# Kernel tuning notes

Measured on AMD Instinct MI355X. Metric: run time of the kernel, lower is better.

Reference implementation:

```python
import jax, jax.numpy as jnp
import numpy as np

V, N = 3, 32768
C2, C3 = 256, 32          # feat_ch_2D, feat_ch_3D
H = W = 128               # 2D feature map size
D = 32                    # 3D volume feature size
CIN = C2 + C3             # 288, MLP in_channels


def setup_inputs() -> dict:
    key = jax.random.key(0)
    ks = jax.random.split(key, 16)
    sc = 0.02
    inp = {
        'pts': jax.random.uniform(ks[0], (1, N, 3), minval=-0.5, maxval=0.5),
        'pts_proj': jax.random.uniform(ks[1], (1, N, 2), minval=-1.0, maxval=1.0),
        'img_feat0': jax.random.normal(ks[2], (V, C2, H, W)),
        'img_feat1': jax.random.normal(ks[3], (V, C2, H, W)),
        'vol_feat0': jax.random.normal(ks[4], (V, C3, D, D, D)),
        'vol_feat1': jax.random.normal(ks[5], (V, C3, D, D, D)),
        'W0': jax.random.normal(ks[6], (1024, CIN)) * sc,  'b0': jnp.zeros((1024,)),
        'W1': jax.random.normal(ks[7], (512, CIN + 1024)) * sc, 'b1': jnp.zeros((512,)),
        'W2': jax.random.normal(ks[8], (256, CIN + 512)) * sc,  'b2': jnp.zeros((256,)),
        'W3': jax.random.normal(ks[9], (128, CIN + 256)) * sc,  'b3': jnp.zeros((128,)),
        'W4': jax.random.normal(ks[10], (1, 128)) * sc,         'b4': jnp.zeros((1,)),
        'mean_num': 3,
    }
    return inp


def _gs2d(feat, gx, gy):
    # feat: [C,H,W]; gx,gy: [N] normalized coords in [-1,1]
    C, Hh, Ww = feat.shape
    ix = jnp.clip(((gx + 1.0) * Ww - 1.0) * 0.5, 0.0, Ww - 1.0)  # align_corners=False, border pad
    iy = jnp.clip(((gy + 1.0) * Hh - 1.0) * 0.5, 0.0, Hh - 1.0)
    x0f, y0f = jnp.floor(ix), jnp.floor(iy)
    wx, wy = ix - x0f, iy - y0f
    x0 = x0f.astype(jnp.int32); x1 = jnp.minimum(x0 + 1, Ww - 1)
    y0 = y0f.astype(jnp.int32); y1 = jnp.minimum(y0 + 1, Hh - 1)
    v00 = feat[:, y0, x0]; v01 = feat[:, y0, x1]
    v10 = feat[:, y1, x0]; v11 = feat[:, y1, x1]
    return (v00 * (1 - wy) * (1 - wx) + v01 * (1 - wy) * wx
            + v10 * wy * (1 - wx) + v11 * wy * wx)  # [C,N]


def _gs3d(feat, gx, gy, gz):
    # feat: [C,D,H,W]; grid x->W, y->H, z->D (torch grid_sample convention)
    C, Dd, Hh, Ww = feat.shape
    ix = jnp.clip(((gx + 1.0) * Ww - 1.0) * 0.5, 0.0, Ww - 1.0)
    iy = jnp.clip(((gy + 1.0) * Hh - 1.0) * 0.5, 0.0, Hh - 1.0)
    iz = jnp.clip(((gz + 1.0) * Dd - 1.0) * 0.5, 0.0, Dd - 1.0)
    x0f, y0f, z0f = jnp.floor(ix), jnp.floor(iy), jnp.floor(iz)
    wx, wy, wz = ix - x0f, iy - y0f, iz - z0f
    x0 = x0f.astype(jnp.int32); x1 = jnp.minimum(x0 + 1, Ww - 1)
    y0 = y0f.astype(jnp.int32); y1 = jnp.minimum(y0 + 1, Hh - 1)
    z0 = z0f.astype(jnp.int32); z1 = jnp.minimum(z0 + 1, Dd - 1)
    def g(zi, yi, xi):
        return feat[:, zi, yi, xi]  # [C,N]
    out = (g(z0, y0, x0) * (1 - wz) * (1 - wy) * (1 - wx)
           + g(z0, y0, x1) * (1 - wz) * (1 - wy) * wx
           + g(z0, y1, x0) * (1 - wz) * wy * (1 - wx)
           + g(z0, y1, x1) * (1 - wz) * wy * wx
           + g(z1, y0, x0) * wz * (1 - wy) * (1 - wx)
           + g(z1, y0, x1) * wz * (1 - wy) * wx
           + g(z1, y1, x0) * wz * wy * (1 - wx)
           + g(z1, y1, x1) * wz * wy * wx)
    return out  # [C,N]


def _lrelu(x):
    return jnp.where(x >= 0, x, 0.2 * x)


def _conv1x1(Wm, bm, x):
    # x: [V,C,N] -> [V,O,N]
    return jnp.einsum('oc,vcn->von', Wm, x) + bm[None, :, None]


def _mlp0(x, W0, b0, W1, b1, W2, b2, W3, b3):
    out = _lrelu(_conv1x1(W0, b0, x))
    out = _lrelu(_conv1x1(W1, b1, jnp.concatenate([x, out], axis=1)))
    out = _lrelu(_conv1x1(W2, b2, jnp.concatenate([x, out], axis=1)))
    out = _lrelu(_conv1x1(W3, b3, jnp.concatenate([x, out], axis=1)))
    return out  # [V,128,N]


def _forward(pts, pts_proj, img_feats, vol_feats,
             W0, b0, W1, b1, W2, b2, W3, b3, W4, b4, mean_num):
    v = img_feats[0].shape[0]
    gx2 = jnp.broadcast_to(pts_proj[:, :, 0], (v, pts_proj.shape[1]))
    gy2 = jnp.broadcast_to(pts_proj[:, :, 1], (v, pts_proj.shape[1]))
    p = pts * 2.0  # pts *= 2.0 before 3D sampling
    gx3 = jnp.broadcast_to(p[:, :, 0], (v, p.shape[1]))
    gy3 = jnp.broadcast_to(p[:, :, 1], (v, p.shape[1]))
    gz3 = jnp.broadcast_to(p[:, :, 2], (v, p.shape[1]))
    outs = []
    for img_feat, vol_feat in zip(img_feats, vol_feats):
        f2 = jax.vmap(_gs2d)(img_feat, gx2, gy2)            # [V,C2,N]
        f3 = jax.vmap(_gs3d)(vol_feat, gx3, gy3, gz3)       # [V,C3,N]
        pt_feat = jnp.concatenate([f2, f3], axis=1)         # [V,288,N]
        pt_out0 = _mlp0(pt_feat, W0, b0, W1, b1, W2, b2, W3, b3)
        pt_out0_mean = jnp.mean(pt_out0[:mean_num], axis=0, keepdims=True)  # [1,128,N]
        sdf = jax.nn.sigmoid(_conv1x1(W4, b4, pt_out0_mean))                # [1,1,N]
        outs.append(jnp.transpose(sdf, (0, 2, 1)))                          # [1,N,1]
    return tuple(outs)


def reference(pts, pts_proj, img_feat0, img_feat1, vol_feat0, vol_feat1,
              W0, b0, W1, b1, W2, b2, W3, b3, W4, b4, mean_num):
    return _forward(pts, pts_proj, [img_feat0, img_feat1], [vol_feat0, vol_feat1],
                    W0, b0, W1, b1, W2, b2, W3, b3, W4, b4, mean_num)
```

## Files before the change

kernel.cpp:

```cpp
#include <hip/hip_runtime.h>
#include <hip/hip_bf16.h>

#define NV 3
#define NPTS 32768
#define C2C 256
#define C3C 32
#define CINC 288
#define CINP 320
#define HH 128
#define WWW 128
#define DDD 32

typedef short bh8 __attribute__((ext_vector_type(8)));
typedef float fx4 __attribute__((ext_vector_type(4)));
typedef unsigned short us4 __attribute__((ext_vector_type(4)));

__device__ __forceinline__ float b2f(unsigned short u) {
    unsigned int x = ((unsigned int)u) << 16;
    return __uint_as_float(x);
}
__device__ __forceinline__ unsigned short f2b(float f) {
    unsigned int x = __float_as_uint(f);
    unsigned int r = (x + 0x7FFFu + ((x >> 16) & 1u)) >> 16;
    return (unsigned short)r;
}

__device__ __forceinline__ void gl2lds16(const unsigned short* g, unsigned short* l) {
    __builtin_amdgcn_global_load_lds(
        (const __attribute__((address_space(1))) unsigned int*)g,
        (__attribute__((address_space(3))) unsigned int*)l, 16, 0, 0);
}

__device__ __forceinline__ int xcd_swz(int orig, int nwg) {
    int xcd = orig & 7;
    int q = nwg >> 3, r = nwg & 7;
    int base = (xcd < r) ? xcd * (q + 1) : r * (q + 1) + (xcd - r) * q;
    return base + (orig >> 3);
}

__global__ void k_wpad(const float* __restrict__ src, unsigned short* __restrict__ dst, int M, int Kp) {
    int idx = blockIdx.x * 256 + threadIdx.x;
    if (idx >= M * Kp) return;
    int m = idx / Kp, k = idx - m * Kp;
    int Ksrc = Kp - 32;
    float v;
    if (k < CINC) v = src[(size_t)m * Ksrc + k];
    else if (k < CINP) v = 0.0f;
    else v = src[(size_t)m * Ksrc + (k - 32)];
    dst[idx] = f2b(v);
}

__global__ void k_timg(const float* __restrict__ in, unsigned short* __restrict__ out) {
    int v = blockIdx.x >> 7, y = blockIdx.x & 127;
    int x0 = blockIdx.y << 6, c0 = blockIdx.z << 6;
    __shared__ float t[64][65];
    int tx = threadIdx.x & 63, tg = threadIdx.x >> 6;
    const float* src = in + (((size_t)(v * C2C + c0) * HH + y) * WWW + x0);
#pragma unroll
    for (int i = 0; i < 16; i++) {
        int cl = tg * 16 + i;
        t[cl][tx] = src[(size_t)cl * (HH * WWW) + tx];
    }
    __syncthreads();
    unsigned short* dst = out + ((size_t)(v * HH + y) * WWW + x0) * C2C + c0;
#pragma unroll
    for (int i = 0; i < 16; i++) {
        int xl = tg * 16 + i;
        dst[(size_t)xl * C2C + tx] = f2b(t[tx][xl]);
    }
}

__global__ void k_tvol(const float* __restrict__ in, unsigned short* __restrict__ out) {
    int v = blockIdx.x;
    int s0 = blockIdx.y << 8;
    __shared__ float t[32][257];
    int tid = threadIdx.x;
    const float* src = in + (size_t)v * C3C * 32768 + s0;
#pragma unroll
    for (int c = 0; c < 32; c++) t[c][tid] = src[(size_t)c * 32768 + tid];
    __syncthreads();
    unsigned short* dst = out + ((size_t)v * 32768 + s0) * C3C;
    int c = tid & 31, sb = tid >> 5;
#pragma unroll
    for (int j = 0; j < 32; j++) {
        int sl = j * 8 + sb;
        dst[(size_t)sl * C3C + c] = f2b(t[c][sl]);
    }
}

__global__ __launch_bounds__(256) void k_sample(const float* __restrict__ pts, const float* __restrict__ proj,
                         const unsigned short* __restrict__ imgT, const unsigned short* __restrict__ volT,
                         unsigned short* __restrict__ ptT, int n0, int Nk) {
    int w = threadIdx.x >> 6, l = threadIdx.x & 63;
    int i = blockIdx.x * 4 + w;
    int v = blockIdx.y;
    int n = n0 + i;
    unsigned short* dstRow = ptT + (size_t)(v * Nk + i) * CINP;

    {
        float gx = proj[n * 2 + 0], gy = proj[n * 2 + 1];
        float ix = fminf(fmaxf(((gx + 1.0f) * (float)WWW - 1.0f) * 0.5f, 0.0f), (float)(WWW - 1));
        float iy = fminf(fmaxf(((gy + 1.0f) * (float)HH - 1.0f) * 0.5f, 0.0f), (float)(HH - 1));
        float x0f = floorf(ix), y0f = floorf(iy);
        float wx = ix - x0f, wy = iy - y0f;
        int x0 = (int)x0f, y0 = (int)y0f;
        int x1 = min(x0 + 1, WWW - 1), y1 = min(y0 + 1, HH - 1);
        const unsigned short* base = imgT + (size_t)v * HH * WWW * C2C;
        us4 a = *((const us4*)(base + ((size_t)(y0 * WWW + x0)) * C2C) + l);
        us4 b = *((const us4*)(base + ((size_t)(y0 * WWW + x1)) * C2C) + l);
        us4 c = *((const us4*)(base + ((size_t)(y1 * WWW + x0)) * C2C) + l);
        us4 d = *((const us4*)(base + ((size_t)(y1 * WWW + x1)) * C2C) + l);
        float w00 = (1.0f - wy) * (1.0f - wx), w01 = (1.0f - wy) * wx;
        float w10 = wy * (1.0f - wx), w11 = wy * wx;
        us4 rv;
#pragma unroll
        for (int r = 0; r < 4; r++) {
            float f = b2f(a[r]) * w00 + b2f(b[r]) * w01 + b2f(c[r]) * w10 + b2f(d[r]) * w11;
            rv[r] = f2b(f);
        }
        *(us4*)(dstRow + l * 4) = rv;
    }
    {
        float gx = pts[n * 3 + 0] * 2.0f, gy = pts[n * 3 + 1] * 2.0f, gz = pts[n * 3 + 2] * 2.0f;
        float ix = fminf(fmaxf(((gx + 1.0f) * (float)DDD - 1.0f) * 0.5f, 0.0f), (float)(DDD - 1));
        float iy = fminf(fmaxf(((gy + 1.0f) * (float)DDD - 1.0f) * 0.5f, 0.0f), (float)(DDD - 1));
        float iz = fminf(fmaxf(((gz + 1.0f) * (float)DDD - 1.0f) * 0.5f, 0.0f), (float)(DDD - 1));
        float x0f = floorf(ix), y0f = floorf(iy), z0f = floorf(iz);
        float wx = ix - x0f, wy = iy - y0f, wz = iz - z0f;
        int x0 = (int)x0f, y0 = (int)y0f, z0 = (int)z0f;
        int x1 = min(x0 + 1, DDD - 1), y1 = min(y0 + 1, DDD - 1), z1 = min(z0 + 1, DDD - 1);
        int c = l & 31, zs = l >> 5;
        int zi = zs ? z1 : z0;
        float wzs = zs ? wz : (1.0f - wz);
        const unsigned short* base = volT + (size_t)v * 32768 * C3C;
        float f00 = b2f(base[((size_t)((zi * 32 + y0) * 32 + x0)) * C3C + c]);
        float f01 = b2f(base[((size_t)((zi * 32 + y0) * 32 + x1)) * C3C + c]);
        float f10 = b2f(base[((size_t)((zi * 32 + y1) * 32 + x0)) * C3C + c]);
        float f11 = b2f(base[((size_t)((zi * 32 + y1) * 32 + x1)) * C3C + c]);
        float r = (f00 * (1.0f - wy) * (1.0f - wx) + f01 * (1.0f - wy) * wx +
                   f10 * wy * (1.0f - wx) + f11 * wy * wx) * wzs;
        float other = __shfl_xor(r, 32);
        r += other;
        if (zs == 0) dstRow[C2C + c] = f2b(r);
    }
    if (l < 8) *(us4*)(dstRow + CINC + l * 4) = (us4){0, 0, 0, 0};
}

template <int K1, int K2, int M>
__device__ __forceinline__ void gemm128_body(const unsigned short* __restrict__ A,
                                             const unsigned short* __restrict__ B1,
                                             const unsigned short* __restrict__ B2,
                                             const float* __restrict__ bias,
                                             unsigned short* __restrict__ C) {
    constexpr int K = K1 + K2;
    __shared__ unsigned short Ash[128 * 32];
    __shared__ unsigned short Bsh[128 * 32];
    int tid = threadIdx.x;
    int w = tid >> 6, l = tid & 63;
    int la = l & 15, lg = l >> 4;
    int wm = w & 1, wn = w >> 1;
    int gx = gridDim.x;
    int nwg = gx * gridDim.y;
    int bid = xcd_swz(blockIdx.y * gx + blockIdx.x, nwg);
    int mBlk = (bid % gx) * 128;
    int nBlk = (bid / gx) * 128;

    int sRow = l >> 2;
    int sCol = (l & 3) * 8;

    fx4 acc[4][4];
#pragma unroll
    for (int mi = 0; mi < 4; mi++)
#pragma unroll
        for (int ni = 0; ni < 4; ni++) acc[mi][ni] = (fx4){0.f, 0.f, 0.f, 0.f};

    const unsigned short* Ag = A + (size_t)mBlk * K;
    {
        const unsigned short* Bg = B1 + (size_t)nBlk * K1;
        for (int k0 = 0; k0 < K1; k0 += 32) {
#pragma unroll
            for (int j = 0; j < 2; j++) {
                int r = w * 32 + j * 16 + sRow;
                gl2lds16(Ag + (size_t)r * K + k0 + sCol, &Ash[r * 32 + sCol]);
                gl2lds16(Bg + (size_t)r * K1 + k0 + sCol, &Bsh[r * 32 + sCol]);
            }
            __syncthreads();
            bh8 af[4], bfv[4];
#pragma unroll
            for (int mi = 0; mi < 4; mi++) af[mi] = *(const bh8*)&Ash[(wm * 64 + mi * 16 + la) * 32 + lg * 8];
#pragma unroll
            for (int ni = 0; ni < 4; ni++) bfv[ni] = *(const bh8*)&Bsh[(wn * 64 + ni * 16 + la) * 32 + lg * 8];
#pragma unroll
            for (int mi = 0; mi < 4; mi++)
#pragma unroll
                for (int ni = 0; ni < 4; ni++)
                    acc[mi][ni] = __builtin_amdgcn_mfma_f32_16x16x32_bf16(af[mi], bfv[ni], acc[mi][ni], 0, 0, 0);
            __syncthreads();
        }
    }
    if constexpr (K2 > 0) {
        const unsigned short* Bg = B2 + (size_t)nBlk * K2;
        for (int k0 = 0; k0 < K2; k0 += 32) {
#pragma unroll
            for (int j = 0; j < 2; j++) {
                int r = w * 32 + j * 16 + sRow;
                gl2lds16(Ag + (size_t)r * K + K1 + k0 + sCol, &Ash[r * 32 + sCol]);
                gl2lds16(Bg + (size_t)r * K2 + k0 + sCol, &Bsh[r * 32 + sCol]);
            }
            __syncthreads();
            bh8 af[4], bfv[4];
#pragma unroll
            for (int mi = 0; mi < 4; mi++) af[mi] = *(const bh8*)&Ash[(wm * 64 + mi * 16 + la) * 32 + lg * 8];
#pragma unroll
            for (int ni = 0; ni < 4; ni++) bfv[ni] = *(const bh8*)&Bsh[(wn * 64 + ni * 16 + la) * 32 + lg * 8];
#pragma unroll
            for (int mi = 0; mi < 4; mi++)
#pragma unroll
                for (int ni = 0; ni < 4; ni++)
                    acc[mi][ni] = __builtin_amdgcn_mfma_f32_16x16x32_bf16(af[mi], bfv[ni], acc[mi][ni], 0, 0, 0);
            __syncthreads();
        }
    }

#pragma unroll
    for (int mi = 0; mi < 4; mi++) {
        int m0 = mBlk + wm * 64 + mi * 16 + lg * 4;
        fx4 bb = *(const fx4*)(bias + m0);
#pragma unroll
        for (int ni = 0; ni < 4; ni++) {
            int n = nBlk + wn * 64 + ni * 16 + la;
            us4 rv;
#pragma unroll
            for (int r = 0; r < 4; r++) {
                float x = acc[mi][ni][r] + bb[r];
                x = (x >= 0.0f) ? x : 0.2f * x;
                rv[r] = f2b(x);
            }
            *(us4*)(C + (size_t)n * M + m0) = rv;
        }
    }
}

__global__ __launch_bounds__(256) void k_g0(const unsigned short* __restrict__ A, const unsigned short* __restrict__ B1,
                                            const float* __restrict__ bias, unsigned short* __restrict__ C) {
    gemm128_body<320, 0, 1024>(A, B1, nullptr, bias, C);
}
__global__ __launch_bounds__(256) void k_g2(const unsigned short* __restrict__ A, const unsigned short* __restrict__ B1,
                                            const unsigned short* __restrict__ B2, const float* __restrict__ bias,
                                            unsigned short* __restrict__ C) {
    gemm128_body<320, 512, 256>(A, B1, B2, bias, C);
}
__global__ __launch_bounds__(256) void k_g3(const unsigned short* __restrict__ A, const unsigned short* __restrict__ B1,
                                            const unsigned short* __restrict__ B2, const float* __restrict__ bias,
                                            unsigned short* __restrict__ C) {
    gemm128_body<320, 256, 128>(A, B1, B2, bias, C);
}

__global__ __launch_bounds__(512) void k_g1(const unsigned short* __restrict__ A,
                                            const unsigned short* __restrict__ B1,
                                            const unsigned short* __restrict__ B2,
                                            const float* __restrict__ bias,
                                            unsigned short* __restrict__ C) {
    constexpr int Kp = 1344;
    constexpr int K2 = 1024;
    constexpr int M = 512;
    constexpr int nt = Kp >> 6;
    __shared__ unsigned short As[2][256 * 64];
    __shared__ unsigned short Bs[2][256 * 64];
    int tid = threadIdx.x;
    int w = tid >> 6, l = tid & 63;
    int la = l & 15, lg = l >> 4;
    int wm = w >> 2, wn = w & 3;
    int g = wn >> 1;
    int gx = gridDim.x;
    int nwg = gx * gridDim.y;
    int bid = xcd_swz(blockIdx.y * gx + blockIdx.x, nwg);
    int mBlk = (bid % gx) * 256;
    int nBlk = (bid / gx) * 256;

    const unsigned short* Ag = A + (size_t)mBlk * Kp;

    fx4 acc[8][4];
#pragma unroll
    for (int mi = 0; mi < 8; mi++)
#pragma unroll
        for (int ni = 0; ni < 4; ni++) acc[mi][ni] = (fx4){0.f, 0.f, 0.f, 0.f};

    auto burst = [&](int t, int nxt) {
        const unsigned short* bsrc;
        size_t ldb;
        int kc;
        if (t < 5) { bsrc = B1; ldb = CINP; kc = t * 64; }
        else       { bsrc = B2; ldb = (size_t)K2; kc = (t - 5) * 64; }
        bsrc += (size_t)nBlk * ldb + kc;
        const unsigned short* asrc = Ag + t * 64;
#pragma unroll
        for (int h = 0; h < 2; h++)
#pragma unroll
            for (int j = 0; j < 2; j++) {
                int idx = j * 512 + tid;
                int r = (h << 7) + (idx >> 3);
                int c = (idx & 7) ^ (r & 7);
                gl2lds16(asrc + (size_t)r * Kp + c * 8, &As[nxt][(h << 13) + idx * 8]);
            }
#pragma unroll
        for (int h = 0; h < 2; h++)
#pragma unroll
            for (int j = 0; j < 2; j++) {
                int idx = j * 512 + tid;
                int r = (h << 7) + (idx >> 3);
                int c = (idx & 7) ^ (r & 7);
                gl2lds16(bsrc + (size_t)r * ldb + c * 8, &Bs[nxt][(h << 13) + idx * 8]);
            }
    };

    burst(0, 0);
    for (int t = 0; t < nt; t++) {
        int cur = t & 1;
        if (t + 1 < nt) {
            burst(t + 1, cur ^ 1);
            if (g == 0) asm volatile("s_waitcnt vmcnt(10)" ::: "memory");
            else        asm volatile("s_waitcnt vmcnt(8)" ::: "memory");
        } else {
            if (g == 0) asm volatile("s_waitcnt vmcnt(2)" ::: "memory");
            else        asm volatile("s_waitcnt vmcnt(0)" ::: "memory");
        }
        const unsigned short* Ab = &As[cur][0];
        const unsigned short* Bb = &Bs[cur][0];
        bh8 afr[4][2];
#pragma unroll
        for (int p = 0; p < 4; p++) {
            int qm = p >> 1, qn = p & 1;
            if (qn == 0) {
#pragma unroll
                for (int m2 = 0; m2 < 4; m2++)
#pragma unroll
                    for (int s = 0; s < 2; s++) {
                        int row = wm * 128 + (qm * 4 + m2) * 16 + la;
                        int c = (s * 4 + lg) ^ (row & 7);
                        afr[m2][s] = *(const bh8*)&Ab[row * 64 + c * 8];
                    }
            }
            bh8 bfr[2][2];
#pragma unroll
            for (int n2 = 0; n2 < 2; n2++)
#pragma unroll
                for (int s = 0; s < 2; s++) {
                    int row = wn * 64 + (qn * 2 + n2) * 16 + la;
                    int c = (s * 4 + lg) ^ (row & 7);
                    bfr[n2][s] = *(const bh8*)&Bb[row * 64 + c * 8];
                }
            __builtin_amdgcn_s_barrier();
            __builtin_amdgcn_s_setprio(1);
#pragma unroll
            for (int m2 = 0; m2 < 4; m2++)
#pragma unroll
                for (int n2 = 0; n2 < 2; n2++)
#pragma unroll
                    for (int s = 0; s < 2; s++)
                        acc[qm * 4 + m2][qn * 2 + n2] = __builtin_amdgcn_mfma_f32_16x16x32_bf16(
                            afr[m2][s], bfr[n2][s], acc[qm * 4 + m2][qn * 2 + n2], 0, 0, 0);
            __builtin_amdgcn_s_setprio(0);
            if (p == 3) asm volatile("s_waitcnt lgkmcnt(0)" ::: "memory");
            __builtin_amdgcn_s_barrier();
        }
    }

#pragma unroll
    for (int mi = 0; mi < 8; mi++) {
        int m0 = mBlk + wm * 128 + mi * 16 + lg * 4;
        fx4 bb = *(const fx4*)(bias + m0);
#pragma unroll
        for (int ni = 0; ni < 4; ni++) {
            int n = nBlk + wn * 64 + ni * 16 + la;
            us4 rv;
#pragma unroll
            for (int r = 0; r < 4; r++) {
                float x = acc[mi][ni][r] + bb[r];
                x = (x >= 0.0f) ? x : 0.2f * x;
                rv[r] = f2b(x);
            }
            *(us4*)(C + (size_t)n * M + m0) = rv;
        }
    }
}

__global__ void k_head(const unsigned short* __restrict__ o3, const float* __restrict__ W4,
                       const float* __restrict__ b4, const int* __restrict__ mn_p,
                       float* __restrict__ out, int n0, int Nk, int level) {
    int i = blockIdx.x * 256 + threadIdx.x;
    if (i >= Nk) return;
    int mn = *mn_p;
    if (mn > NV) mn = NV;
    if (mn < 1) mn = 1;
    float s = 0.0f;
    for (int v = 0; v < mn; v++) {
        const unsigned short* row = o3 + (size_t)(v * Nk + i) * 128;
        for (int c0 = 0; c0 < 128; c0 += 8) {
            bh8 x = *(const bh8*)(row + c0);
#pragma unroll
            for (int r = 0; r < 8; r++) s += W4[c0 + r] * b2f((unsigned short)x[r]);
        }
    }
    s = s / (float)mn + b4[0];
    out[(size_t)level * NPTS + n0 + i] = 1.0f / (1.0f + expf(-s));
}

extern "C" void kernel_launch(void* const* d_in, const int* in_sizes, int n_in,
                              void* d_out, int out_size, void* d_ws, size_t ws_size,
                              hipStream_t stream) {
    const float* pts = (const float*)d_in[0];
    const float* proj = (const float*)d_in[1];
    const float* img[2] = {(const float*)d_in[2], (const float*)d_in[3]};
    const float* vol[2] = {(const float*)d_in[4], (const float*)d_in[5]};
    const float* Wf[4] = {(const float*)d_in[6], (const float*)d_in[8], (const float*)d_in[10], (const float*)d_in[12]};
    const float* bf[4] = {(const float*)d_in[7], (const float*)d_in[9], (const float*)d_in[11], (const float*)d_in[13]};
    const float* W4 = (const float*)d_in[14];
    const float* b4 = (const float*)d_in[15];
    const int* mn = (const int*)d_in[16];
    float* out = (float*)d_out;

    const int Kp[4] = {320, 1344, 832, 576};
    const int Msz[4] = {1024, 512, 256, 128};

    char* ws = (char*)d_ws;
    size_t off = 0;
    auto alloc = [&](size_t bytes) -> char* {
        char* p = ws + off;
        off = (off + bytes + 255) & ~(size_t)255;
        return p;
    };

    unsigned short* Wb[4];
    for (int i = 0; i < 4; i++) Wb[i] = (unsigned short*)alloc((size_t)Msz[i] * Kp[i] * 2);
    unsigned short* imgT = (unsigned short*)alloc((size_t)NV * HH * WWW * C2C * 2);
    unsigned short* volT = (unsigned short*)alloc((size_t)NV * 32768 * C3C * 2);
    size_t fixed = off;

    const size_t perPt = (size_t)NV * 2 * (CINP + 1024 + 512 + 256 + 128);
    int Nk = NPTS;
    if (fixed + (size_t)Nk * perPt + 4096 > ws_size) {
        size_t avail = (ws_size > fixed + 4096) ? (ws_size - fixed - 4096) : 0;
        long nk = (long)(avail / perPt);
        nk = (nk / 256) * 256;
        if (nk < 256) nk = 256;
        if (nk > NPTS) nk = NPTS;
        Nk = (int)nk;
    }
    unsigned short* ptT = (unsigned short*)alloc((size_t)NV * Nk * CINP * 2);
    unsigned short* o0 = (unsigned short*)alloc((size_t)NV * Nk * 1024 * 2);
    unsigned short* o1 = (unsigned short*)alloc((size_t)NV * Nk * 512 * 2);
    unsigned short* o2 = (unsigned short*)alloc((size_t)NV * Nk * 256 * 2);
    unsigned short* o3 = (unsigned short*)alloc((size_t)NV * Nk * 128 * 2);

    for (int i = 0; i < 4; i++) {
        int n = Msz[i] * Kp[i];
        k_wpad<<<(n + 255) / 256, 256, 0, stream>>>(Wf[i], Wb[i], Msz[i], Kp[i]);
    }

    for (int lvl = 0; lvl < 2; lvl++) {
        k_timg<<<dim3(NV * HH, WWW / 64, C2C / 64), 256, 0, stream>>>(img[lvl], imgT);
        k_tvol<<<dim3(NV, 32768 / 256), 256, 0, stream>>>(vol[lvl], volT);
        for (int n0 = 0; n0 < NPTS; n0 += Nk) {
            int nk = NPTS - n0 < Nk ? NPTS - n0 : Nk;
            int NC = NV * nk;
            k_sample<<<dim3(nk / 4, NV), 256, 0, stream>>>(pts, proj, imgT, volT, ptT, n0, nk);
            k_g0<<<dim3(1024 / 128, NC / 128), 256, 0, stream>>>(Wb[0], ptT, bf[0], o0);
            k_g1<<<dim3(512 / 256, NC / 256), 512, 0, stream>>>(Wb[1], ptT, o0, bf[1], o1);
            k_g2<<<dim3(256 / 128, NC / 128), 256, 0, stream>>>(Wb[2], ptT, o1, bf[2], o2);
            k_g3<<<dim3(128 / 128, NC / 128), 256, 0, stream>>>(Wb[3], ptT, o2, bf[3], o3);
            k_head<<<(nk + 255) / 256, 256, 0, stream>>>(o3, W4, b4, mn, out, n0, nk, lvl);
        }
    }
}
```

Before: 1.079 ms.

## Reschedule k_g1 prefetch, split its launch in halves, parallelize head reduction

The k_g1 GEMM now issues the next tile's global-to-LDS burst after the first MFMA sub-step instead of before compute, with one uniform vmcnt wait before the final barrier. It is also launched as two half-grid kernels using a column offset. The head kernel now gives each point 16 lanes, each doing a slice of the 128-channel dot product, then combines them with a shuffle reduction, so more threads run and loads coalesce. Splitting k_g1 adds a launch and may leave the GPU partly idle at the tail, and the new wait placement changes load/compute overlap.

```diff
diff --git a/kernel.cpp b/kernel.cpp
--- a/kernel.cpp
+++ b/kernel.cpp
@@ -260,7 +260,7 @@
                                             const unsigned short* __restrict__ B1,
                                             const unsigned short* __restrict__ B2,
                                             const float* __restrict__ bias,
-                                            unsigned short* __restrict__ C) {
+                                            unsigned short* __restrict__ C, int nOff) {
     constexpr int Kp = 1344;
     constexpr int K2 = 1024;
     constexpr int M = 512;
@@ -271,12 +271,11 @@
     int w = tid >> 6, l = tid & 63;
     int la = l & 15, lg = l >> 4;
     int wm = w >> 2, wn = w & 3;
-    int g = wn >> 1;
     int gx = gridDim.x;
     int nwg = gx * gridDim.y;
     int bid = xcd_swz(blockIdx.y * gx + blockIdx.x, nwg);
     int mBlk = (bid % gx) * 256;
-    int nBlk = (bid / gx) * 256;
+    int nBlk = (bid / gx) * 256 + nOff;
 
     const unsigned short* Ag = A + (size_t)mBlk * Kp;
 
@@ -315,16 +314,10 @@
     };
 
     burst(0, 0);
+    asm volatile("s_waitcnt vmcnt(0)" ::: "memory");
+    __builtin_amdgcn_s_barrier();
     for (int t = 0; t < nt; t++) {
         int cur = t & 1;
-        if (t + 1 < nt) {
-            burst(t + 1, cur ^ 1);
-            if (g == 0) asm volatile("s_waitcnt vmcnt(10)" ::: "memory");
-            else        asm volatile("s_waitcnt vmcnt(8)" ::: "memory");
-        } else {
-            if (g == 0) asm volatile("s_waitcnt vmcnt(2)" ::: "memory");
-            else        asm volatile("s_waitcnt vmcnt(0)" ::: "memory");
-        }
         const unsigned short* Ab = &As[cur][0];
         const unsigned short* Bb = &Bs[cur][0];
         bh8 afr[4][2];
@@ -361,7 +354,11 @@
                         acc[qm * 4 + m2][qn * 2 + n2] = __builtin_amdgcn_mfma_f32_16x16x32_bf16(
                             afr[m2][s], bfr[n2][s], acc[qm * 4 + m2][qn * 2 + n2], 0, 0, 0);
             __builtin_amdgcn_s_setprio(0);
-            if (p == 3) asm volatile("s_waitcnt lgkmcnt(0)" ::: "memory");
+            if (p == 0 && t + 1 < nt) burst(t + 1, cur ^ 1);
+            if (p == 3) {
+                asm volatile("s_waitcnt lgkmcnt(0)" ::: "memory");
+                if (t + 1 < nt) asm volatile("s_waitcnt vmcnt(8)" ::: "memory");
+            }
             __builtin_amdgcn_s_barrier();
         }
     }
@@ -385,25 +382,32 @@
     }
 }
 
-__global__ void k_head(const unsigned short* __restrict__ o3, const float* __restrict__ W4,
+__global__ __launch_bounds__(256) void k_head(const unsigned short* __restrict__ o3, const float* __restrict__ W4,
                        const float* __restrict__ b4, const int* __restrict__ mn_p,
                        float* __restrict__ out, int n0, int Nk, int level) {
-    int i = blockIdx.x * 256 + threadIdx.x;
+    int wv = threadIdx.x >> 6, l = threadIdx.x & 63;
+    int sub = l >> 4, cl = l & 15;
+    int i = blockIdx.x * 16 + wv * 4 + sub;
     if (i >= Nk) return;
     int mn = *mn_p;
     if (mn > NV) mn = NV;
     if (mn < 1) mn = 1;
+    fx4 w0 = *(const fx4*)(W4 + cl * 8);
+    fx4 w1 = *(const fx4*)(W4 + cl * 8 + 4);
     float s = 0.0f;
     for (int v = 0; v < mn; v++) {
-        const unsigned short* row = o3 + (size_t)(v * Nk + i) * 128;
-        for (int c0 = 0; c0 < 128; c0 += 8) {
-            bh8 x = *(const bh8*)(row + c0);
-#pragma unroll
-            for (int r = 0; r < 8; r++) s += W4[c0 + r] * b2f((unsigned short)x[r]);
-        }
-    }
-    s = s / (float)mn + b4[0];
-    out[(size_t)level * NPTS + n0 + i] = 1.0f / (1.0f + expf(-s));
+        bh8 x = *(const bh8*)(o3 + (size_t)(v * Nk + i) * 128 + cl * 8);
+#pragma unroll
+        for (int r = 0; r < 4; r++) s += w0[r] * b2f((unsigned short)x[r]);
+#pragma unroll
+        for (int r = 0; r < 4; r++) s += w1[r] * b2f((unsigned short)x[4 + r]);
+    }
+#pragma unroll
+    for (int m = 1; m < 16; m <<= 1) s += __shfl_xor(s, m);
+    if (cl == 0) {
+        s = s / (float)mn + b4[0];
+        out[(size_t)level * NPTS + n0 + i] = 1.0f / (1.0f + expf(-s));
+    }
 }
 
 extern "C" void kernel_launch(void* const* d_in, const int* in_sizes, int n_in,
@@ -442,8 +446,8 @@
     if (fixed + (size_t)Nk * perPt + 4096 > ws_size) {
         size_t avail = (ws_size > fixed + 4096) ? (ws_size - fixed - 4096) : 0;
         long nk = (long)(avail / perPt);
-        nk = (nk / 256) * 256;
-        if (nk < 256) nk = 256;
+        nk = (nk / 512) * 512;
+        if (nk < 512) nk = 512;
         if (nk > NPTS) nk = NPTS;
         Nk = (int)nk;
     }
@@ -464,12 +468,14 @@
         for (int n0 = 0; n0 < NPTS; n0 += Nk) {
             int nk = NPTS - n0 < Nk ? NPTS - n0 : Nk;
             int NC = NV * nk;
+            int NH = NC / 2;
             k_sample<<<dim3(nk / 4, NV), 256, 0, stream>>>(pts, proj, imgT, volT, ptT, n0, nk);
             k_g0<<<dim3(1024 / 128, NC / 128), 256, 0, stream>>>(Wb[0], ptT, bf[0], o0);
-            k_g1<<<dim3(512 / 256, NC / 256), 512, 0, stream>>>(Wb[1], ptT, o0, bf[1], o1);
+            k_g1<<<dim3(512 / 256, NH / 256), 512, 0, stream>>>(Wb[1], ptT, o0, bf[1], o1, 0);
+            k_g1<<<dim3(512 / 256, NH / 256), 512, 0, stream>>>(Wb[1], ptT, o0, bf[1], o1, NH);
             k_g2<<<dim3(256 / 128, NC / 128), 256, 0, stream>>>(Wb[2], ptT, o1, bf[2], o2);
             k_g3<<<dim3(128 / 128, NC / 128), 256, 0, stream>>>(Wb[3], ptT, o2, bf[3], o3);
-            k_head<<<(nk + 255) / 256, 256, 0, stream>>>(o3, W4, b4, mn, out, n0, nk, lvl);
-        }
-    }
-}
+            k_head<<<(nk + 15) / 16, 256, 0, stream>>>(o3, W4, b4, mn, out, n0, nk, lvl);
+        }
+    }
+}
```

After: 1.089 ms. No clear change (+0.9%).
